# Kernel optimization log

Hardware: AMD Instinct MI355X
Metric: run time of the kernel (lower is better)

The kernel has to match this reference:

```python
import jax, jax.numpy as jnp
import numpy as np

B, D_IN, FD = 32768, 2048, 128
N1 = N2 = N3 = 4
T = 1.0  # temperature buffer value (eval mode)
LN_EPS = 1e-5

def _gelu(x):
    return jax.nn.gelu(x, approximate=False)  # torch nn.GELU default = exact erf

def setup_inputs() -> dict:
    key = jax.random.key(0)
    ks = iter(jax.random.split(key, 64))
    def rn(shape, s=0.02):
        return jax.random.normal(next(ks), shape, jnp.float32) * s
    inp = {"x": jax.random.normal(next(ks), (B, D_IN), jnp.float32)}
    # input_proj: Linear(2048,512) GELU Linear(512,256) LayerNorm(256)
    inp.update(ipW1=rn((D_IN, 512)), ipb1=jnp.zeros(512), ipW2=rn((512, 256)), ipb2=jnp.zeros(256),
               ln_g=jnp.ones(256), ln_b=jnp.zeros(256))
    def level(din, nc, pfx):
        return {pfx+"W3d": rn((din, 3)), pfx+"b3d": jnp.zeros(3),
                pfx+"c": rn((nc, 3), 0.3), pfx+"lr": jnp.zeros(nc),
                pfx+"f1W": rn((din, FD)), pfx+"f1b": jnp.zeros(FD),
                pfx+"f2W": rn((FD, FD)), pfx+"f2b": jnp.zeros(FD),
                pfx+"rW": rn((FD+3, nc)), pfx+"rb": jnp.zeros(nc)}
    inp.update(level(256, N1, "l1"))
    inp.update(level(FD, N2, "l2"))
    inp.update(level(FD, N3, "l3"))
    # expert_head: Linear(128+4+4+4, 256) GELU Linear(256, 64)
    inp.update(ehW1=rn((FD+N1+N2+N3, 256)), ehb1=jnp.zeros(256),
               ehW2=rn((256, N1*N2*N3)), ehb2=jnp.zeros(N1*N2*N3))
    return inp

def _level_fwd(x, W3d, b3d, c, f1W, f1b, f2W, f2b, rW, rb):
    # x: (B, din) -> probs (B, nc), features (B, FD)
    pos = x @ W3d + b3d                                   # (B, 3)
    d_sq = ((pos[:, None, :] - c[None, :, :]) ** 2).sum(-1)  # (B, nc)
    geo = -d_sq / (2.0 * T * T + 1e-8)                    # non-spectral geo signal
    feat = _gelu(x @ f1W + f1b) @ f2W + f2b               # (B, FD)
    logits = jnp.concatenate([feat, pos], axis=-1) @ rW + rb + 0.5 * geo
    probs = jax.nn.softmax(logits / max(T, 0.1), axis=-1)  # eval path: plain softmax
    return probs, feat

def _router_fwd(x, ipW1, ipb1, ipW2, ipb2, ln_g, ln_b,
                l1W3d, l1b3d, l1c, l1f1W, l1f1b, l1f2W, l1f2b, l1rW, l1rb,
                l2W3d, l2b3d, l2c, l2f1W, l2f1b, l2f2W, l2f2b, l2rW, l2rb,
                l3W3d, l3b3d, l3c, l3f1W, l3f1b, l3f2W, l3f2b, l3rW, l3rb,
                ehW1, ehb1, ehW2, ehb2):
    h = _gelu(x @ ipW1 + ipb1) @ ipW2 + ipb2
    mu = h.mean(-1, keepdims=True)
    var = ((h - mu) ** 2).mean(-1, keepdims=True)
    h = (h - mu) * jax.lax.rsqrt(var + LN_EPS) * ln_g + ln_b  # LayerNorm(256)
    p1, f1 = _level_fwd(h,  l1W3d, l1b3d, l1c, l1f1W, l1f1b, l1f2W, l1f2b, l1rW, l1rb)
    p2, f2 = _level_fwd(f1, l2W3d, l2b3d, l2c, l2f1W, l2f1b, l2f2W, l2f2b, l2rW, l2rb)
    p3, f3 = _level_fwd(f2, l3W3d, l3b3d, l3c, l3f1W, l3f1b, l3f2W, l3f2b, l3rW, l3rb)
    combined = jnp.concatenate([f3, p1, p2, p3], axis=-1)  # (B, 140)
    logits = _gelu(combined @ ehW1 + ehb1) @ ehW2 + ehb2   # (B, 64)
    expert_probs = jax.nn.softmax(logits / max(T, 0.1), axis=-1)
    return expert_probs

def reference(x, ipW1, ipb1, ipW2, ipb2, ln_g, ln_b,
              l1W3d, l1b3d, l1c, l1lr, l1f1W, l1f1b, l1f2W, l1f2b, l1rW, l1rb,
              l2W3d, l2b3d, l2c, l2lr, l2f1W, l2f1b, l2f2W, l2f2b, l2rW, l2rb,
              l3W3d, l3b3d, l3c, l3lr, l3f1W, l3f1b, l3f2W, l3f2b, l3rW, l3rb,
              ehW1, ehb1, ehW2, ehb2):
    # l?lr (log_radii) are unused in non-spectral mode, matching the source.
    expert_probs = _router_fwd(x, ipW1, ipb1, ipW2, ipb2, ln_g, ln_b,
                               l1W3d, l1b3d, l1c, l1f1W, l1f1b, l1f2W, l1f2b, l1rW, l1rb,
                               l2W3d, l2b3d, l2c, l2f1W, l2f1b, l2f2W, l2f2b, l2rW, l2rb,
                               l3W3d, l3b3d, l3c, l3f1W, l3f1b, l3f2W, l3f2b, l3rW, l3rb,
                               ehW1, ehb1, ehW2, ehb2)
    expert_ids = jnp.argmax(expert_probs, axis=-1)
    return expert_probs, expert_ids
```

## Files before the change

kernel.cpp:

```cpp
#include <hip/hip_runtime.h>
#include <hip/hip_bf16.h>
#include <cstdint>
#include <cstddef>


typedef short  s8v  __attribute__((ext_vector_type(8)));
typedef float  f4v  __attribute__((ext_vector_type(4)));
typedef float  f16v __attribute__((ext_vector_type(16)));
typedef unsigned int u32;

#define B_ROWS 32768

__device__ inline short f2bf(float x) {
    __hip_bfloat16 h = __float2bfloat16(x);
    return __builtin_bit_cast(short, h);
}
__device__ inline float bf2f(short s) {
    return __bfloat162float(__builtin_bit_cast(__hip_bfloat16, s));
}
__device__ inline float gelu_f(float x) {
    return 0.5f * x * (1.0f + erff(x * 0.70710678118654752440f));
}
__device__ inline void gload_lds16(const short* g, short* l) {
    __builtin_amdgcn_global_load_lds(
        (const __attribute__((address_space(1))) u32*)g,
        (__attribute__((address_space(3))) u32*)l, 16, 0, 0);
}

__global__ void split_w1_img(const float* __restrict__ W, short* __restrict__ img)
{
    const int idx = blockIdx.x * 256 + threadIdx.x;
    const int p = idx & 7;
    const int n = (idx >> 3) & 511;
    const int t = idx >> 12;
    const int cs = p ^ (n & 7);
    const int plane = cs >> 2, kc = cs & 3;
    const int kbase = t * 32 + kc * 8;
    s8v v8;
    #pragma unroll
    for (int e = 0; e < 8; ++e) {
        const float v = W[(size_t)(kbase + e) * 512 + n];
        const short h = f2bf(v);
        v8[e] = plane ? f2bf(v - bf2f(h)) : h;
    }
    *(s8v*)&img[(size_t)((t * 512 + n) * 64 + p * 8)] = v8;
}

__launch_bounds__(256, 4)
__global__ void gemm1k(const float* __restrict__ X,
                       const short* __restrict__ Bimg,
                       const float* __restrict__ bias,
                       float* __restrict__ out)
{
    __shared__ short smem[128 * 64 * 2];
    short* Ab = smem;
    short* Bb = smem + 128 * 64;

    const int tid = threadIdx.x;
    const int l = tid & 63, wid = tid >> 6;
    const int wr = wid >> 1, wc = wid & 1;

    const int d = blockIdx.x;
    const int xcd = d & 7;
    const int m0 = ((xcd & 1) * 128 + (d >> 3)) * 128;
    const int n0 = (xcd >> 1) * 128;

    const int ar = tid & 127, ah = tid >> 7;
    const float* xP = X + (size_t)(m0 + ar) * 2048 + ah * 16;
    short* awr = Ab + ar * 64;
    const int pw0 = ((ah * 2    ) ^ (ar & 7)) * 8;
    const int pw1 = ((ah * 2 + 1) ^ (ar & 7)) * 8;
    const int pw2 = ((ah * 2 + 4) ^ (ar & 7)) * 8;
    const int pw3 = ((ah * 2 + 5) ^ (ar & 7)) * 8;

    const short* bP = Bimg + (size_t)n0 * 64 + (size_t)(wid * 4) * 512 + (size_t)l * 8;
    short* bD = Bb + wid * 4 * 512;

    f16v acc[2][2];
    #pragma unroll
    for (int m = 0; m < 2; ++m)
        #pragma unroll
        for (int n = 0; n < 2; ++n) acc[m][n] = (f16v)0.0f;

    f4v cur0, cur1, cur2, cur3;
    cur0 = *(const f4v*)(xP + 0);
    cur1 = *(const f4v*)(xP + 4);
    cur2 = *(const f4v*)(xP + 8);
    cur3 = *(const f4v*)(xP + 12);

    for (int t = 0; t < 64; ++t) {
        s8v hi0, hi1, lo0, lo1;
        #pragma unroll
        for (int e = 0; e < 4; ++e) {
            float v;
            short h;
            v = cur0[e]; h = f2bf(v); hi0[e]     = h; lo0[e]     = f2bf(v - bf2f(h));
            v = cur1[e]; h = f2bf(v); hi0[e + 4] = h; lo0[e + 4] = f2bf(v - bf2f(h));
            v = cur2[e]; h = f2bf(v); hi1[e]     = h; lo1[e]     = f2bf(v - bf2f(h));
            v = cur3[e]; h = f2bf(v); hi1[e + 4] = h; lo1[e + 4] = f2bf(v - bf2f(h));
        }
        __syncthreads();
        *(s8v*)&awr[pw0] = hi0;
        *(s8v*)&awr[pw1] = hi1;
        *(s8v*)&awr[pw2] = lo0;
        *(s8v*)&awr[pw3] = lo1;
        {
            const short* bt = bP + (size_t)t * 32768;
            gload_lds16(bt,          bD);
            gload_lds16(bt +  512,   bD + 512);
            gload_lds16(bt + 1024,   bD + 1024);
            gload_lds16(bt + 1536,   bD + 1536);
        }
        if (t < 63) {
            const float* p = xP + (t + 1) * 32;
            cur0 = *(const f4v*)(p + 0);
            cur1 = *(const f4v*)(p + 4);
            cur2 = *(const f4v*)(p + 8);
            cur3 = *(const f4v*)(p + 12);
        }
        __syncthreads();

        #pragma unroll
        for (int ks = 0; ks < 2; ++ks) {
            const int ph0 = ks * 2 + (l >> 5);
            s8v ahf[2], alf[2], bhf[2], blf[2];
            #pragma unroll
            for (int m = 0; m < 2; ++m) {
                const int row = wr * 64 + m * 32 + (l & 31);
                const int ph = ph0 ^ (row & 7);
                ahf[m] = *(const s8v*)&Ab[row * 64 + ph * 8];
                alf[m] = *(const s8v*)&Ab[row * 64 + (ph ^ 4) * 8];
            }
            #pragma unroll
            for (int n = 0; n < 2; ++n) {
                const int col = wc * 64 + n * 32 + (l & 31);
                const int ph = ph0 ^ (col & 7);
                bhf[n] = *(const s8v*)&Bb[col * 64 + ph * 8];
                blf[n] = *(const s8v*)&Bb[col * 64 + (ph ^ 4) * 8];
            }
            #pragma unroll
            for (int m = 0; m < 2; ++m)
                #pragma unroll
                for (int n = 0; n < 2; ++n) {
                    acc[m][n] = __builtin_amdgcn_mfma_f32_32x32x16_bf16(ahf[m], bhf[n], acc[m][n], 0, 0, 0);
                    acc[m][n] = __builtin_amdgcn_mfma_f32_32x32x16_bf16(ahf[m], blf[n], acc[m][n], 0, 0, 0);
                    acc[m][n] = __builtin_amdgcn_mfma_f32_32x32x16_bf16(alf[m], bhf[n], acc[m][n], 0, 0, 0);
                }
        }
    }

    #pragma unroll
    for (int m = 0; m < 2; ++m) {
        #pragma unroll
        for (int n = 0; n < 2; ++n) {
            const int gcol = n0 + wc * 64 + n * 32 + (l & 31);
            const float bv = bias[gcol];
            #pragma unroll
            for (int r = 0; r < 16; ++r) {
                const int grow = m0 + wr * 64 + m * 32
                               + (r & 3) + 8 * (r >> 2) + 4 * (l >> 5);
                out[(size_t)grow * 512 + gcol] = gelu_f(acc[m][n][r] + bv);
            }
        }
    }
}

struct SplitDesc { const float* W; short* dst; int K, N, Kpad, blk0; };
struct SplitPack { SplitDesc d[9]; };

__global__ void split_all(SplitPack p) {
    const int bid = blockIdx.x;
    int i = 0;
    #pragma unroll
    for (int j = 1; j < 9; ++j) if (bid >= p.d[j].blk0) i = j;
    const SplitDesc& D = p.d[i];
    const int idx = (bid - D.blk0) * 256 + threadIdx.x;
    const int total = D.N * D.Kpad;
    if (idx >= total) return;
    const int n = idx / D.Kpad, k = idx - n * D.Kpad;
    const float v = (k < D.K) ? D.W[(size_t)k * D.N + n] : 0.0f;
    const short hs = f2bf(v);
    D.dst[idx] = hs;
    D.dst[total + idx] = f2bf(v - bf2f(hs));
}

template<int DIN, int OSTR>
__launch_bounds__(256, 2)
__global__ void levelk(const float* __restrict__ X,
                       const short* __restrict__ Wa, const float* __restrict__ ba,
                       const short* __restrict__ Wb, const float* __restrict__ bb,
                       float* __restrict__ F)
{
    constexpr int NT1 = DIN / 32;
    __shared__ short stepb[(64 + 128) * 64];
    __shared__ float gb[64 * 132];
    short* Ab = stepb;
    short* Bb = stepb + 64 * 64;

    const int tid = threadIdx.x;
    const int l = tid & 63, wid = tid >> 6;
    const int wr = wid >> 1, wc = wid & 1;
    const int m0 = blockIdx.x * 64;

    const int ar = tid >> 2, aseg = tid & 3;
    short* aw = Ab + ar * 64;
    const int ps0 = ((aseg    ) ^ (ar & 7)) * 8;
    const int ps1 = ((aseg + 4) ^ (ar & 7)) * 8;

    const int cs = (l & 7) ^ (l >> 3);
    const int bplane = cs >> 2, kslot = cs & 3;

    f16v acc[2];
    acc[0] = (f16v)0.0f; acc[1] = (f16v)0.0f;

    auto computeStep = [&]() {
        #pragma unroll
        for (int ks = 0; ks < 2; ++ks) {
            const int c0 = ks * 2 + (l >> 5);
            const int row = wr * 32 + (l & 31);
            const int pa = c0 ^ (row & 7);
            s8v ah = *(const s8v*)&Ab[row * 64 + pa * 8];
            s8v al = *(const s8v*)&Ab[row * 64 + (pa ^ 4) * 8];
            #pragma unroll
            for (int n = 0; n < 2; ++n) {
                const int col = wc * 64 + n * 32 + (l & 31);
                const int pb = c0 ^ (col & 7);
                s8v bh = *(const s8v*)&Bb[col * 64 + pb * 8];
                s8v bl = *(const s8v*)&Bb[col * 64 + (pb ^ 4) * 8];
                acc[n] = __builtin_amdgcn_mfma_f32_32x32x16_bf16(ah, bh, acc[n], 0, 0, 0);
                acc[n] = __builtin_amdgcn_mfma_f32_32x32x16_bf16(ah, bl, acc[n], 0, 0, 0);
                acc[n] = __builtin_amdgcn_mfma_f32_32x32x16_bf16(al, bh, acc[n], 0, 0, 0);
            }
        }
    };
    auto cvt = [&](const f4v& u, const f4v& w, s8v& hi, s8v& lo) {
        #pragma unroll
        for (int e = 0; e < 4; ++e) {
            short h;
            h = f2bf(u[e]); hi[e]     = h; lo[e]     = f2bf(u[e] - bf2f(h));
            h = f2bf(w[e]); hi[e + 4] = h; lo[e + 4] = f2bf(w[e] - bf2f(h));
        }
    };

    {
        const float* xP = X + (size_t)(m0 + ar) * DIN + aseg * 8;
        f4v cA = *(const f4v*)(xP);
        f4v cB = *(const f4v*)(xP + 4);
        for (int t = 0; t < NT1; ++t) {
            s8v hi, lo; cvt(cA, cB, hi, lo);
            __syncthreads();
            *(s8v*)&aw[ps0] = hi;
            *(s8v*)&aw[ps1] = lo;
            #pragma unroll
            for (int j = 0; j < 4; ++j) {
                const int col = (wid * 4 + j) * 8 + (l >> 3);
                gload_lds16(Wa + (size_t)bplane * (128 * DIN) + (size_t)col * DIN
                               + t * 32 + kslot * 8,
                            Bb + (wid * 4 + j) * 512);
            }
            if (t + 1 < NT1) {
                const float* p = xP + (t + 1) * 32;
                cA = *(const f4v*)(p);
                cB = *(const f4v*)(p + 4);
            }
            __syncthreads();
            computeStep();
        }
    }

    #pragma unroll
    for (int n = 0; n < 2; ++n) {
        const int col = wc * 64 + n * 32 + (l & 31);
        const float bv = ba[col];
        #pragma unroll
        for (int r = 0; r < 16; ++r) {
            const int row = wr * 32 + (r & 3) + 8 * (r >> 2) + 4 * (l >> 5);
            gb[row * 132 + col] = gelu_f(acc[n][r] + bv);
        }
    }
    acc[0] = (f16v)0.0f; acc[1] = (f16v)0.0f;
    __syncthreads();

    {
        const float* gP = gb + ar * 132 + aseg * 8;
        f4v cA = *(const f4v*)(gP);
        f4v cB = *(const f4v*)(gP + 4);
        for (int t = 0; t < 4; ++t) {
            s8v hi, lo; cvt(cA, cB, hi, lo);
            __syncthreads();
            *(s8v*)&aw[ps0] = hi;
            *(s8v*)&aw[ps1] = lo;
            #pragma unroll
            for (int j = 0; j < 4; ++j) {
                const int col = (wid * 4 + j) * 8 + (l >> 3);
                gload_lds16(Wb + (size_t)bplane * (128 * 128) + (size_t)col * 128
                               + t * 32 + kslot * 8,
                            Bb + (wid * 4 + j) * 512);
            }
            if (t + 1 < 4) {
                const float* p = gP + (t + 1) * 32;
                cA = *(const f4v*)(p);
                cB = *(const f4v*)(p + 4);
            }
            __syncthreads();
            computeStep();
        }
    }

    #pragma unroll
    for (int n = 0; n < 2; ++n) {
        const int col = wc * 64 + n * 32 + (l & 31);
        const float bv = bb[col];
        #pragma unroll
        for (int r = 0; r < 16; ++r) {
            const int row = wr * 32 + (r & 3) + 8 * (r >> 2) + 4 * (l >> 5);
            F[(size_t)(m0 + row) * OSTR + col] = acc[n][r] + bv;
        }
    }
}

template<int BM, int BN, int EPI>
__launch_bounds__(256, 2)
__global__ void gemm32(const float* __restrict__ A, int lda,
                       const short* __restrict__ Bsp, int ldb, int NK,
                       const float* __restrict__ bias, int K, int N, int ntiles,
                       float* __restrict__ out, float* __restrict__ out2,
                       const float* __restrict__ lng, const float* __restrict__ lnb)
{
    constexpr int MF  = BM / 64;
    constexpr int NFw = BN / 64;
    constexpr int BUF = (BM + BN) * 64;
    constexpr int FPT = BM / 8;
    constexpr int TPR = 32 / FPT;
    constexpr int nBI = BN / 32;
    __shared__ short smem[2 * BUF];

    const int tid = threadIdx.x;
    const int l   = tid & 63, wid = tid >> 6;
    const int wr  = wid >> 1, wc = wid & 1;
    const int bid = blockIdx.x;
    const int ntb = bid % ntiles, mtb = bid / ntiles;
    const int m0  = mtb * BM, n0 = ntb * BN;

    const int ar = tid / TPR, aseg = tid % TPR;
    const float* aP = A + (size_t)(m0 + ar) * lda + aseg * FPT;

    const short* bg[nBI];
    {
        const int cs = (l & 7) ^ (l >> 3);
        const int plane = cs >> 2, kslot = cs & 3;
        #pragma unroll
        for (int j = 0; j < nBI; ++j) {
            const int col = (wid * nBI + j) * 8 + (l >> 3);
            bg[j] = Bsp + (size_t)plane * NK + (size_t)(n0 + col) * ldb + kslot * 8;
        }
    }

    f16v acc[MF][NFw];
    #pragma unroll
    for (int m = 0; m < MF; ++m)
        #pragma unroll
        for (int n = 0; n < NFw; ++n) acc[m][n] = (f16v)0.0f;

    f4v areg[FPT / 4];

    auto loadA = [&](int t) {
        const float* p = aP + t * 32;
        #pragma unroll
        for (int i = 0; i < FPT / 4; ++i) areg[i] = *(const f4v*)(p + i * 4);
    };
    auto stageB = [&](int t, short* buf) {
        short* Bb = buf + BM * 64;
        #pragma unroll
        for (int j = 0; j < nBI; ++j)
            gload_lds16(bg[j] + t * 32, Bb + (wid * nBI + j) * 512);
    };
    auto writeA = [&](short* buf) {
        #pragma unroll
        for (int c = 0; c < FPT / 8; ++c) {
            s8v hi, lo;
            #pragma unroll
            for (int e = 0; e < 8; ++e) {
                const float v = areg[c * 2 + (e >> 2)][e & 3];
                const short hs = f2bf(v);
                hi[e] = hs; lo[e] = f2bf(v - bf2f(hs));
            }
            const int csh = aseg * (FPT / 8) + c;
            *(s8v*)&buf[ar * 64 + ((csh    ) ^ (ar & 7)) * 8] = hi;
            *(s8v*)&buf[ar * 64 + ((csh + 4) ^ (ar & 7)) * 8] = lo;
        }
    };
    auto compute = [&](const short* buf) {
        const short* Ab = buf;
        const short* Bb = buf + BM * 64;
        #pragma unroll
        for (int ks = 0; ks < 2; ++ks) {
            const int csb = ks * 2 + (l >> 5);
            s8v ah[MF], al[MF], bh[NFw], bl[NFw];
            #pragma unroll
            for (int m = 0; m < MF; ++m) {
                const int row = wr * (BM / 2) + m * 32 + (l & 31);
                ah[m] = *(const s8v*)&Ab[row * 64 + ((csb    ) ^ (row & 7)) * 8];
                al[m] = *(const s8v*)&Ab[row * 64 + ((csb + 4) ^ (row & 7)) * 8];
            }
            #pragma unroll
            for (int n = 0; n < NFw; ++n) {
                const int col = wc * (BN / 2) + n * 32 + (l & 31);
                bh[n] = *(const s8v*)&Bb[col * 64 + ((csb    ) ^ (col & 7)) * 8];
                bl[n] = *(const s8v*)&Bb[col * 64 + ((csb + 4) ^ (col & 7)) * 8];
            }
            __builtin_amdgcn_s_setprio(1);
            #pragma unroll
            for (int m = 0; m < MF; ++m)
                #pragma unroll
                for (int n = 0; n < NFw; ++n) {
                    acc[m][n] = __builtin_amdgcn_mfma_f32_32x32x16_bf16(ah[m], bh[n], acc[m][n], 0, 0, 0);
                    acc[m][n] = __builtin_amdgcn_mfma_f32_32x32x16_bf16(ah[m], bl[n], acc[m][n], 0, 0, 0);
                    acc[m][n] = __builtin_amdgcn_mfma_f32_32x32x16_bf16(al[m], bh[n], acc[m][n], 0, 0, 0);
                }
            __builtin_amdgcn_s_setprio(0);
        }
    };

    const int NT = K / 32;
    loadA(0);
    stageB(0, smem);
    writeA(smem);
    __syncthreads();
    for (int t = 0; t < NT; ++t) {
        short* curb = smem + (t & 1) * BUF;
        short* nxtb = smem + ((t & 1) ^ 1) * BUF;
        const bool pf = (t + 1 < NT);
        if (pf) { loadA(t + 1); stageB(t + 1, nxtb); }
        compute(curb);
        if (pf) writeA(nxtb);
        __syncthreads();
    }

    if constexpr (EPI <= 1) {
        #pragma unroll
        for (int m = 0; m < MF; ++m) {
            #pragma unroll
            for (int n = 0; n < NFw; ++n) {
                const int gcol = n0 + wc * (BN / 2) + n * 32 + (l & 31);
                const float bv = bias[gcol];
                #pragma unroll
                for (int r = 0; r < 16; ++r) {
                    const int grow = m0 + wr * (BM / 2) + m * 32
                                   + (r & 3) + 8 * (r >> 2) + 4 * (l >> 5);
                    float xv = acc[m][n][r] + bv;
                    if constexpr (EPI == 0) xv = gelu_f(xv);
                    out[(size_t)grow * N + gcol] = xv;
                }
            }
        }
    } else if constexpr (EPI == 2) {
        float* LT = reinterpret_cast<float*>(smem);
        const int gcolL = wc * 32 + (l & 31);
        const float bv = bias[gcolL];
        #pragma unroll
        for (int r = 0; r < 16; ++r) {
            const int row = wr * 32 + (r & 3) + 8 * (r >> 2) + 4 * (l >> 5);
            LT[row * 64 + gcolL] = acc[0][0][r] + bv;
        }
        __syncthreads();
        const int r = tid >> 2, q = tid & 3;
        const float* Lr = LT + r * 64 + q * 16;
        float mx = Lr[0];
        #pragma unroll
        for (int c = 1; c < 16; ++c) mx = fmaxf(mx, Lr[c]);
        mx = fmaxf(mx, __shfl_xor(mx, 1));
        mx = fmaxf(mx, __shfl_xor(mx, 2));
        float ev[16]; float s = 0.0f;
        #pragma unroll
        for (int c = 0; c < 16; ++c) { ev[c] = expf(Lr[c] - mx); s += ev[c]; }
        s += __shfl_xor(s, 1);
        s += __shfl_xor(s, 2);
        float pmax = -1.0f; int arg = 0;
        #pragma unroll
        for (int c = 0; c < 16; ++c) {
            const float pv = ev[c] / s;
            out[(size_t)(m0 + r) * 64 + q * 16 + c] = pv;
            if (pv > pmax) { pmax = pv; arg = q * 16 + c; }
        }
        #pragma unroll
        for (int off = 1; off <= 2; off <<= 1) {
            const float po = __shfl_xor(pmax, off);
            const int   ao = __shfl_xor(arg, off);
            if (po > pmax || (po == pmax && ao < arg)) { pmax = po; arg = ao; }
        }
        if (q == 0) out2[m0 + r] = (float)arg;
    } else {
        float* LT = reinterpret_cast<float*>(smem);
        #pragma unroll
        for (int n = 0; n < NFw; ++n) {
            const int col = wc * (BN / 2) + n * 32 + (l & 31);
            const float bv = bias[col];
            #pragma unroll
            for (int r = 0; r < 16; ++r) {
                const int row = wr * 32 + (r & 3) + 8 * (r >> 2) + 4 * (l >> 5);
                LT[row * 264 + col] = acc[0][n][r] + bv;
            }
        }
        __syncthreads();
        const int r = tid >> 2, q = tid & 3;
        const float* Lr = LT + r * 264 + q * 64;
        float s = 0.0f;
        #pragma unroll
        for (int i = 0; i < 64; ++i) s += Lr[i];
        s += __shfl_xor(s, 1);
        s += __shfl_xor(s, 2);
        const float mu = s * 0.00390625f;
        float qv = 0.0f;
        #pragma unroll
        for (int i = 0; i < 64; ++i) { const float dd = Lr[i] - mu; qv += dd * dd; }
        qv += __shfl_xor(qv, 1);
        qv += __shfl_xor(qv, 2);
        const float sc = 1.0f / sqrtf(qv * 0.00390625f + 1e-5f);
        #pragma unroll
        for (int i = 0; i < 64; ++i) {
            const int c = q * 64 + i;
            out[(size_t)(m0 + r) * 256 + c] = (Lr[i] - mu) * sc * lng[c] + lnb[c];
        }
    }
}

__global__ __launch_bounds__(256) void p_kernel(
    const float* __restrict__ X, int din,
    const float* __restrict__ F, int fstr,
    const float* __restrict__ W3d, const float* __restrict__ b3d,
    const float* __restrict__ cc,
    const float* __restrict__ rW, const float* __restrict__ rb,
    float* __restrict__ Pout)
{
    const int row = blockIdx.x * 4 + (threadIdx.x >> 6);
    const int l   = threadIdx.x & 63;
    float px0 = 0.f, px1 = 0.f, px2 = 0.f;
    const int per = din >> 6;
    const float* xr = X + (size_t)row * din;
    for (int i = 0; i < per; ++i) {
        const int k = l + (i << 6);
        const float xv = xr[k];
        px0 += xv * W3d[k*3 + 0];
        px1 += xv * W3d[k*3 + 1];
        px2 += xv * W3d[k*3 + 2];
    }
    float g0 = 0.f, g1 = 0.f, g2 = 0.f, g3 = 0.f;
    const float* fr = F + (size_t)row * fstr;
    #pragma unroll
    for (int i = 0; i < 2; ++i) {
        const int k = l + (i << 6);
        const float fv = fr[k];
        g0 += fv * rW[k*4 + 0]; g1 += fv * rW[k*4 + 1];
        g2 += fv * rW[k*4 + 2]; g3 += fv * rW[k*4 + 3];
    }
    #pragma unroll
    for (int o = 32; o; o >>= 1) {
        px0 += __shfl_xor(px0, o); px1 += __shfl_xor(px1, o); px2 += __shfl_xor(px2, o);
        g0  += __shfl_xor(g0, o);  g1  += __shfl_xor(g1, o);
        g2  += __shfl_xor(g2, o);  g3  += __shfl_xor(g3, o);
    }
    if (l == 0) {
        const float pos0 = px0 + b3d[0], pos1 = px1 + b3d[1], pos2 = px2 + b3d[2];
        float lg[4];
        float mx = -1e30f;
        float gg[4] = {g0, g1, g2, g3};
        #pragma unroll
        for (int c = 0; c < 4; ++c) {
            float a = gg[c] + rb[c]
                    + pos0 * rW[512 + c] + pos1 * rW[516 + c] + pos2 * rW[520 + c];
            const float d0 = pos0 - cc[c*3 + 0];
            const float d1 = pos1 - cc[c*3 + 1];
            const float d2 = pos2 - cc[c*3 + 2];
            a += 0.5f * (-(d0*d0 + d1*d1 + d2*d2) / 2.00000001f);
            lg[c] = a;
            mx = fmaxf(mx, a);
        }
        const float e0 = expf(lg[0]-mx), e1 = expf(lg[1]-mx),
                    e2 = expf(lg[2]-mx), e3 = expf(lg[3]-mx);
        const float s = e0 + e1 + e2 + e3;
        float* pr = Pout + (size_t)row * 160;
        pr[0] = e0/s; pr[1] = e1/s; pr[2] = e2/s; pr[3] = e3/s;
    }
}

extern "C" void kernel_launch(void* const* d_in, const int* in_sizes, int n_in,
                              void* d_out, int out_size, void* d_ws, size_t ws_size,
                              hipStream_t stream)
{
    (void)in_sizes; (void)n_in; (void)out_size; (void)ws_size;

    const float* x    = (const float*)d_in[0];
    const float* ipW1 = (const float*)d_in[1];
    const float* ipb1 = (const float*)d_in[2];
    const float* ipW2 = (const float*)d_in[3];
    const float* ipb2 = (const float*)d_in[4];
    const float* ln_g = (const float*)d_in[5];
    const float* ln_b = (const float*)d_in[6];
    const float* W3d[3] = {(const float*)d_in[7],  (const float*)d_in[17], (const float*)d_in[27]};
    const float* b3d[3] = {(const float*)d_in[8],  (const float*)d_in[18], (const float*)d_in[28]};
    const float* cc[3]  = {(const float*)d_in[9],  (const float*)d_in[19], (const float*)d_in[29]};
    const float* f1W[3] = {(const float*)d_in[11], (const float*)d_in[21], (const float*)d_in[31]};
    const float* f1b[3] = {(const float*)d_in[12], (const float*)d_in[22], (const float*)d_in[32]};
    const float* f2W[3] = {(const float*)d_in[13], (const float*)d_in[23], (const float*)d_in[33]};
    const float* f2b[3] = {(const float*)d_in[14], (const float*)d_in[24], (const float*)d_in[34]};
    const float* rW[3]  = {(const float*)d_in[15], (const float*)d_in[25], (const float*)d_in[35]};
    const float* rb[3]  = {(const float*)d_in[16], (const float*)d_in[26], (const float*)d_in[36]};
    const float* ehW1 = (const float*)d_in[37];
    const float* ehb1 = (const float*)d_in[38];
    const float* ehW2 = (const float*)d_in[39];
    const float* ehb2 = (const float*)d_in[40];

    size_t off = 0;
    auto take = [&](size_t bytes) -> void* {
        void* p = (char*)d_ws + off;
        off += (bytes + 255) & ~(size_t)255;
        return p;
    };
    auto takeW = [&](int N, int Kpad) -> short* {
        return (short*)take((size_t)2 * N * Kpad * 2);
    };
    short* W1img = (short*)take((size_t)64 * 512 * 64 * 2);
    short* W2s = takeW(256, 512);
    short* L1a = takeW(128, 256);
    short* L1b = takeW(128, 128);
    short* L2a = takeW(128, 128);
    short* L2b = takeW(128, 128);
    short* L3a = takeW(128, 128);
    short* L3b = takeW(128, 128);
    short* E1s = takeW(256, 160);
    short* E2s = takeW(64, 256);
    float* h1 = (float*)take((size_t)B_ROWS * 512 * 4);
    float* h2 = (float*)take((size_t)B_ROWS * 256 * 4);
    float* f1 = (float*)take((size_t)B_ROWS * 128 * 4);
    float* f2 = (float*)take((size_t)B_ROWS * 128 * 4);
    float* comb = h1;
    float* geh  = (float*)((char*)h1 + ((size_t)22 << 20));

    split_w1_img<<<(64 * 512 * 8) / 256, 256, 0, stream>>>(ipW1, W1img);
    SplitPack sp;
    int blk = 0;
    auto desc = [&](int i, const float* W, short* dst, int K, int N, int Kpad) {
        sp.d[i] = {W, dst, K, N, Kpad, blk};
        blk += (N * Kpad + 255) / 256;
    };
    desc(0, ipW2,   W2s,  512, 256,  512);
    desc(1, f1W[0], L1a,  256, 128,  256);
    desc(2, f2W[0], L1b,  128, 128,  128);
    desc(3, f1W[1], L2a,  128, 128,  128);
    desc(4, f2W[1], L2b,  128, 128,  128);
    desc(5, f1W[2], L3a,  128, 128,  128);
    desc(6, f2W[2], L3b,  128, 128,  128);
    desc(7, ehW1,   E1s,  140, 256,  160);
    desc(8, ehW2,   E2s,  256,  64,  256);
    split_all<<<blk, 256, 0, stream>>>(sp);

    const dim3 blkT(256);
    constexpr int MG64 = B_ROWS / 64;

    gemm1k<<<1024, blkT, 0, stream>>>(x, W1img, ipb1, h1);
    gemm32<64,256,3><<<MG64, blkT, 0, stream>>>(h1, 512, W2s, 512, 256*512, ipb2,
                                                512, 256, 1, h2, nullptr, ln_g, ln_b);

    levelk<256,128><<<MG64, blkT, 0, stream>>>(h2, L1a, f1b[0], L1b, f2b[0], f1);
    p_kernel<<<B_ROWS/4, 256, 0, stream>>>(h2, 256, f1, 128, W3d[0], b3d[0], cc[0], rW[0], rb[0], comb + 128);
    levelk<128,128><<<MG64, blkT, 0, stream>>>(f1, L2a, f1b[1], L2b, f2b[1], f2);
    p_kernel<<<B_ROWS/4, 256, 0, stream>>>(f1, 128, f2, 128, W3d[1], b3d[1], cc[1], rW[1], rb[1], comb + 132);
    levelk<128,160><<<MG64, blkT, 0, stream>>>(f2, L3a, f1b[2], L3b, f2b[2], comb);
    p_kernel<<<B_ROWS/4, 256, 0, stream>>>(f2, 128, comb, 160, W3d[2], b3d[2], cc[2], rW[2], rb[2], comb + 136);

    gemm32<64,128,0><<<MG64*2, blkT, 0, stream>>>(comb, 160, E1s, 160, 256*160, ehb1,
                                                  160, 256, 2, geh, nullptr, nullptr, nullptr);
    gemm32<64,64,2><<<MG64, blkT, 0, stream>>>(geh, 256, E2s, 256, 64*256, ehb2,
                                               256, 64, 1, (float*)d_out,
                                               (float*)d_out + (size_t)B_ROWS * 64, nullptr, nullptr);
}
```

Baseline: 555.5 us.

## Fuse all three router levels and expert-head first layer into one megakernel

Replaces the three levelk launches, three p_kernel launches and the first expert-head GEMM with a single per-64-row kernel. Intermediate features, position/probability results and the combined vector stay in LDS instead of going through global memory. Separately, the second input-projection GEMM now uses a 128x128 tile with a plain bias epilogue, followed by a standalone vectorized LayerNorm kernel instead of the fused LN epilogue. This removes launch overhead and global round-trips between stages, at the cost of heavy register use (a 16-vector register cache of the input row), large LDS usage that may limit occupancy, and an extra pass over h2 for LayerNorm.

New measurement: 538.9 us. -3.0%, faster.

```diff
diff --git a/kernel.cpp b/kernel.cpp
--- a/kernel.cpp
+++ b/kernel.cpp
@@ -10,6 +10,8 @@
 typedef unsigned int u32;
 
 #define B_ROWS 32768
+
+template<int N> struct IC { static constexpr int v = N; };
 
 __device__ inline short f2bf(float x) {
     __hip_bfloat16 h = __float2bfloat16(x);
@@ -184,148 +186,12 @@
     D.dst[total + idx] = f2bf(v - bf2f(hs));
 }
 
-template<int DIN, int OSTR>
-__launch_bounds__(256, 2)
-__global__ void levelk(const float* __restrict__ X,
-                       const short* __restrict__ Wa, const float* __restrict__ ba,
-                       const short* __restrict__ Wb, const float* __restrict__ bb,
-                       float* __restrict__ F)
-{
-    constexpr int NT1 = DIN / 32;
-    __shared__ short stepb[(64 + 128) * 64];
-    __shared__ float gb[64 * 132];
-    short* Ab = stepb;
-    short* Bb = stepb + 64 * 64;
-
-    const int tid = threadIdx.x;
-    const int l = tid & 63, wid = tid >> 6;
-    const int wr = wid >> 1, wc = wid & 1;
-    const int m0 = blockIdx.x * 64;
-
-    const int ar = tid >> 2, aseg = tid & 3;
-    short* aw = Ab + ar * 64;
-    const int ps0 = ((aseg    ) ^ (ar & 7)) * 8;
-    const int ps1 = ((aseg + 4) ^ (ar & 7)) * 8;
-
-    const int cs = (l & 7) ^ (l >> 3);
-    const int bplane = cs >> 2, kslot = cs & 3;
-
-    f16v acc[2];
-    acc[0] = (f16v)0.0f; acc[1] = (f16v)0.0f;
-
-    auto computeStep = [&]() {
-        #pragma unroll
-        for (int ks = 0; ks < 2; ++ks) {
-            const int c0 = ks * 2 + (l >> 5);
-            const int row = wr * 32 + (l & 31);
-            const int pa = c0 ^ (row & 7);
-            s8v ah = *(const s8v*)&Ab[row * 64 + pa * 8];
-            s8v al = *(const s8v*)&Ab[row * 64 + (pa ^ 4) * 8];
-            #pragma unroll
-            for (int n = 0; n < 2; ++n) {
-                const int col = wc * 64 + n * 32 + (l & 31);
-                const int pb = c0 ^ (col & 7);
-                s8v bh = *(const s8v*)&Bb[col * 64 + pb * 8];
-                s8v bl = *(const s8v*)&Bb[col * 64 + (pb ^ 4) * 8];
-                acc[n] = __builtin_amdgcn_mfma_f32_32x32x16_bf16(ah, bh, acc[n], 0, 0, 0);
-                acc[n] = __builtin_amdgcn_mfma_f32_32x32x16_bf16(ah, bl, acc[n], 0, 0, 0);
-                acc[n] = __builtin_amdgcn_mfma_f32_32x32x16_bf16(al, bh, acc[n], 0, 0, 0);
-            }
-        }
-    };
-    auto cvt = [&](const f4v& u, const f4v& w, s8v& hi, s8v& lo) {
-        #pragma unroll
-        for (int e = 0; e < 4; ++e) {
-            short h;
-            h = f2bf(u[e]); hi[e]     = h; lo[e]     = f2bf(u[e] - bf2f(h));
-            h = f2bf(w[e]); hi[e + 4] = h; lo[e + 4] = f2bf(w[e] - bf2f(h));
-        }
-    };
-
-    {
-        const float* xP = X + (size_t)(m0 + ar) * DIN + aseg * 8;
-        f4v cA = *(const f4v*)(xP);
-        f4v cB = *(const f4v*)(xP + 4);
-        for (int t = 0; t < NT1; ++t) {
-            s8v hi, lo; cvt(cA, cB, hi, lo);
-            __syncthreads();
-            *(s8v*)&aw[ps0] = hi;
-            *(s8v*)&aw[ps1] = lo;
-            #pragma unroll
-            for (int j = 0; j < 4; ++j) {
-                const int col = (wid * 4 + j) * 8 + (l >> 3);
-                gload_lds16(Wa + (size_t)bplane * (128 * DIN) + (size_t)col * DIN
-                               + t * 32 + kslot * 8,
-                            Bb + (wid * 4 + j) * 512);
-            }
-            if (t + 1 < NT1) {
-                const float* p = xP + (t + 1) * 32;
-                cA = *(const f4v*)(p);
-                cB = *(const f4v*)(p + 4);
-            }
-            __syncthreads();
-            computeStep();
-        }
-    }
-
-    #pragma unroll
-    for (int n = 0; n < 2; ++n) {
-        const int col = wc * 64 + n * 32 + (l & 31);
-        const float bv = ba[col];
-        #pragma unroll
-        for (int r = 0; r < 16; ++r) {
-            const int row = wr * 32 + (r & 3) + 8 * (r >> 2) + 4 * (l >> 5);
-            gb[row * 132 + col] = gelu_f(acc[n][r] + bv);
-        }
-    }
-    acc[0] = (f16v)0.0f; acc[1] = (f16v)0.0f;
-    __syncthreads();
-
-    {
-        const float* gP = gb + ar * 132 + aseg * 8;
-        f4v cA = *(const f4v*)(gP);
-        f4v cB = *(const f4v*)(gP + 4);
-        for (int t = 0; t < 4; ++t) {
-            s8v hi, lo; cvt(cA, cB, hi, lo);
-            __syncthreads();
-            *(s8v*)&aw[ps0] = hi;
-            *(s8v*)&aw[ps1] = lo;
-            #pragma unroll
-            for (int j = 0; j < 4; ++j) {
-                const int col = (wid * 4 + j) * 8 + (l >> 3);
-                gload_lds16(Wb + (size_t)bplane * (128 * 128) + (size_t)col * 128
-                               + t * 32 + kslot * 8,
-                            Bb + (wid * 4 + j) * 512);
-            }
-            if (t + 1 < 4) {
-                const float* p = gP + (t + 1) * 32;
-                cA = *(const f4v*)(p);
-                cB = *(const f4v*)(p + 4);
-            }
-            __syncthreads();
-            computeStep();
-        }
-    }
-
-    #pragma unroll
-    for (int n = 0; n < 2; ++n) {
-        const int col = wc * 64 + n * 32 + (l & 31);
-        const float bv = bb[col];
-        #pragma unroll
-        for (int r = 0; r < 16; ++r) {
-            const int row = wr * 32 + (r & 3) + 8 * (r >> 2) + 4 * (l >> 5);
-            F[(size_t)(m0 + row) * OSTR + col] = acc[n][r] + bv;
-        }
-    }
-}
-
 template<int BM, int BN, int EPI>
 __launch_bounds__(256, 2)
 __global__ void gemm32(const float* __restrict__ A, int lda,
                        const short* __restrict__ Bsp, int ldb, int NK,
                        const float* __restrict__ bias, int K, int N, int ntiles,
-                       float* __restrict__ out, float* __restrict__ out2,
-                       const float* __restrict__ lng, const float* __restrict__ lnb)
+                       float* __restrict__ out, float* __restrict__ out2)
 {
     constexpr int MF  = BM / 64;
     constexpr int NFw = BN / 64;
@@ -454,7 +320,7 @@
                 }
             }
         }
-    } else if constexpr (EPI == 2) {
+    } else {
         float* LT = reinterpret_cast<float*>(smem);
         const int gcolL = wc * 32 + (l & 31);
         const float bv = bias[gcolL];
@@ -490,97 +356,290 @@
             if (po > pmax || (po == pmax && ao < arg)) { pmax = po; arg = ao; }
         }
         if (q == 0) out2[m0 + r] = (float)arg;
-    } else {
-        float* LT = reinterpret_cast<float*>(smem);
-        #pragma unroll
-        for (int n = 0; n < NFw; ++n) {
-            const int col = wc * (BN / 2) + n * 32 + (l & 31);
-            const float bv = bias[col];
-            #pragma unroll
-            for (int r = 0; r < 16; ++r) {
-                const int row = wr * 32 + (r & 3) + 8 * (r >> 2) + 4 * (l >> 5);
-                LT[row * 264 + col] = acc[0][n][r] + bv;
-            }
-        }
-        __syncthreads();
-        const int r = tid >> 2, q = tid & 3;
-        const float* Lr = LT + r * 264 + q * 64;
-        float s = 0.0f;
-        #pragma unroll
-        for (int i = 0; i < 64; ++i) s += Lr[i];
-        s += __shfl_xor(s, 1);
-        s += __shfl_xor(s, 2);
-        const float mu = s * 0.00390625f;
-        float qv = 0.0f;
-        #pragma unroll
-        for (int i = 0; i < 64; ++i) { const float dd = Lr[i] - mu; qv += dd * dd; }
-        qv += __shfl_xor(qv, 1);
-        qv += __shfl_xor(qv, 2);
-        const float sc = 1.0f / sqrtf(qv * 0.00390625f + 1e-5f);
-        #pragma unroll
-        for (int i = 0; i < 64; ++i) {
-            const int c = q * 64 + i;
-            out[(size_t)(m0 + r) * 256 + c] = (Lr[i] - mu) * sc * lng[c] + lnb[c];
-        }
-    }
-}
-
-__global__ __launch_bounds__(256) void p_kernel(
-    const float* __restrict__ X, int din,
-    const float* __restrict__ F, int fstr,
-    const float* __restrict__ W3d, const float* __restrict__ b3d,
-    const float* __restrict__ cc,
-    const float* __restrict__ rW, const float* __restrict__ rb,
-    float* __restrict__ Pout)
+    }
+}
+
+__global__ __launch_bounds__(256) void ln_kernel(float* __restrict__ H,
+                                                 const float* __restrict__ G,
+                                                 const float* __restrict__ Bv)
 {
     const int row = blockIdx.x * 4 + (threadIdx.x >> 6);
     const int l   = threadIdx.x & 63;
-    float px0 = 0.f, px1 = 0.f, px2 = 0.f;
-    const int per = din >> 6;
-    const float* xr = X + (size_t)row * din;
-    for (int i = 0; i < per; ++i) {
-        const int k = l + (i << 6);
-        const float xv = xr[k];
-        px0 += xv * W3d[k*3 + 0];
-        px1 += xv * W3d[k*3 + 1];
-        px2 += xv * W3d[k*3 + 2];
-    }
-    float g0 = 0.f, g1 = 0.f, g2 = 0.f, g3 = 0.f;
-    const float* fr = F + (size_t)row * fstr;
-    #pragma unroll
-    for (int i = 0; i < 2; ++i) {
-        const int k = l + (i << 6);
-        const float fv = fr[k];
-        g0 += fv * rW[k*4 + 0]; g1 += fv * rW[k*4 + 1];
-        g2 += fv * rW[k*4 + 2]; g3 += fv * rW[k*4 + 3];
-    }
-    #pragma unroll
-    for (int o = 32; o; o >>= 1) {
-        px0 += __shfl_xor(px0, o); px1 += __shfl_xor(px1, o); px2 += __shfl_xor(px2, o);
-        g0  += __shfl_xor(g0, o);  g1  += __shfl_xor(g1, o);
-        g2  += __shfl_xor(g2, o);  g3  += __shfl_xor(g3, o);
-    }
-    if (l == 0) {
-        const float pos0 = px0 + b3d[0], pos1 = px1 + b3d[1], pos2 = px2 + b3d[2];
-        float lg[4];
-        float mx = -1e30f;
-        float gg[4] = {g0, g1, g2, g3};
-        #pragma unroll
-        for (int c = 0; c < 4; ++c) {
-            float a = gg[c] + rb[c]
-                    + pos0 * rW[512 + c] + pos1 * rW[516 + c] + pos2 * rW[520 + c];
-            const float d0 = pos0 - cc[c*3 + 0];
-            const float d1 = pos1 - cc[c*3 + 1];
-            const float d2 = pos2 - cc[c*3 + 2];
-            a += 0.5f * (-(d0*d0 + d1*d1 + d2*d2) / 2.00000001f);
-            lg[c] = a;
-            mx = fmaxf(mx, a);
-        }
-        const float e0 = expf(lg[0]-mx), e1 = expf(lg[1]-mx),
-                    e2 = expf(lg[2]-mx), e3 = expf(lg[3]-mx);
-        const float s = e0 + e1 + e2 + e3;
-        float* pr = Pout + (size_t)row * 160;
-        pr[0] = e0/s; pr[1] = e1/s; pr[2] = e2/s; pr[3] = e3/s;
+    float* hr = H + (size_t)row * 256;
+    f4v v = *reinterpret_cast<const f4v*>(&hr[l * 4]);
+    float s = v[0] + v[1] + v[2] + v[3];
+    #pragma unroll
+    for (int o = 32; o; o >>= 1) s += __shfl_xor(s, o);
+    const float mu = s * 0.00390625f;
+    f4v d = v - mu;
+    float q = d[0]*d[0] + d[1]*d[1] + d[2]*d[2] + d[3]*d[3];
+    #pragma unroll
+    for (int o = 32; o; o >>= 1) q += __shfl_xor(q, o);
+    const float var = q * 0.00390625f;
+    const float sc  = 1.0f / sqrtf(var + 1e-5f);
+    f4v gg = *reinterpret_cast<const f4v*>(&G[l * 4]);
+    f4v bb = *reinterpret_cast<const f4v*>(&Bv[l * 4]);
+    f4v o4 = d * sc * gg + bb;
+    *reinterpret_cast<f4v*>(&hr[l * 4]) = o4;
+}
+
+struct TailArgs {
+    const float* h2;
+    const short* La[3]; const float* ba[3];
+    const short* Lb[3]; const float* bb[3];
+    const short* E1;    const float* eb1;
+    const float* W3d[3]; const float* b3d[3]; const float* cc[3];
+    const float* rW[3];  const float* rb[3];
+    float* geh;
+};
+
+__launch_bounds__(256, 2)
+__global__ void megatail(TailArgs A)
+{
+    __shared__ float Fbuf[64 * 164];
+    __shared__ short Astage[64 * 64];
+    __shared__ short Bstage[128 * 64];
+    __shared__ float pbuf[64 * 12];
+
+    const int tid = threadIdx.x;
+    const int l = tid & 63, wid = tid >> 6;
+    const int wr = wid >> 1, wc = wid & 1;
+    const int m0 = blockIdx.x * 64;
+
+    const int ar = tid >> 2, aseg = tid & 3;
+    short* aw = Astage + ar * 64;
+    const int ps0 = ((aseg    ) ^ (ar & 7)) * 8;
+    const int ps1 = ((aseg + 4) ^ (ar & 7)) * 8;
+
+    const int cs = (l & 7) ^ (l >> 3);
+    const int bplane = cs >> 2, kslot = cs & 3;
+
+    f16v acc[2];
+
+    auto accReset = [&]() { acc[0] = (f16v)0.0f; acc[1] = (f16v)0.0f; };
+
+    auto computeStep = [&]() {
+        #pragma unroll
+        for (int ks = 0; ks < 2; ++ks) {
+            const int c0 = ks * 2 + (l >> 5);
+            const int row = wr * 32 + (l & 31);
+            const int pa = c0 ^ (row & 7);
+            s8v ah = *(const s8v*)&Astage[row * 64 + pa * 8];
+            s8v al = *(const s8v*)&Astage[row * 64 + (pa ^ 4) * 8];
+            #pragma unroll
+            for (int n = 0; n < 2; ++n) {
+                const int col = wc * 64 + n * 32 + (l & 31);
+                const int pb = c0 ^ (col & 7);
+                s8v bh = *(const s8v*)&Bstage[col * 64 + pb * 8];
+                s8v bl = *(const s8v*)&Bstage[col * 64 + (pb ^ 4) * 8];
+                acc[n] = __builtin_amdgcn_mfma_f32_32x32x16_bf16(ah, bh, acc[n], 0, 0, 0);
+                acc[n] = __builtin_amdgcn_mfma_f32_32x32x16_bf16(ah, bl, acc[n], 0, 0, 0);
+                acc[n] = __builtin_amdgcn_mfma_f32_32x32x16_bf16(al, bh, acc[n], 0, 0, 0);
+            }
+        }
+    };
+    auto cvt = [&](const f4v& u, const f4v& w, s8v& hi, s8v& lo) {
+        #pragma unroll
+        for (int e = 0; e < 4; ++e) {
+            short h;
+            h = f2bf(u[e]); hi[e]     = h; lo[e]     = f2bf(u[e] - bf2f(h));
+            h = f2bf(w[e]); hi[e + 4] = h; lo[e + 4] = f2bf(w[e] - bf2f(h));
+        }
+    };
+    auto stageBt = [&](const short* Bpl, int Kpad, int NKpl, int n0, int t) {
+        #pragma unroll
+        for (int j = 0; j < 4; ++j) {
+            const int col = (wid * 4 + j) * 8 + (l >> 3);
+            gload_lds16(Bpl + (size_t)bplane * NKpl + (size_t)(n0 + col) * Kpad
+                            + t * 32 + kslot * 8,
+                        Bstage + (wid * 4 + j) * 512);
+        }
+    };
+
+    auto phaseRegs = [&](auto NTc, const f4v* xr, const short* Bpl, int Kpad, int NKpl) {
+        constexpr int NT = decltype(NTc)::v;
+        #pragma unroll
+        for (int t = 0; t < NT; ++t) {
+            s8v hi, lo; cvt(xr[2 * t], xr[2 * t + 1], hi, lo);
+            __syncthreads();
+            *(s8v*)&aw[ps0] = hi;
+            *(s8v*)&aw[ps1] = lo;
+            stageBt(Bpl, Kpad, NKpl, 0, t);
+            __syncthreads();
+            computeStep();
+        }
+    };
+    auto phaseLDS = [&](auto NTc, const short* Bpl, int Kpad, int NKpl, int n0) {
+        constexpr int NT = decltype(NTc)::v;
+        f4v cA = *(const f4v*)&Fbuf[ar * 164 + aseg * 8];
+        f4v cB = *(const f4v*)&Fbuf[ar * 164 + aseg * 8 + 4];
+        #pragma unroll
+        for (int t = 0; t < NT; ++t) {
+            s8v hi, lo; cvt(cA, cB, hi, lo);
+            __syncthreads();
+            *(s8v*)&aw[ps0] = hi;
+            *(s8v*)&aw[ps1] = lo;
+            stageBt(Bpl, Kpad, NKpl, n0, t);
+            if (t + 1 < NT) {
+                cA = *(const f4v*)&Fbuf[ar * 164 + (t + 1) * 32 + aseg * 8];
+                cB = *(const f4v*)&Fbuf[ar * 164 + (t + 1) * 32 + aseg * 8 + 4];
+            }
+            __syncthreads();
+            computeStep();
+        }
+    };
+    auto outEpi = [&](const float* bv_arr, bool dogelu) {
+        #pragma unroll
+        for (int n = 0; n < 2; ++n) {
+            const int col = wc * 64 + n * 32 + (l & 31);
+            const float bv = bv_arr[col];
+            #pragma unroll
+            for (int r = 0; r < 16; ++r) {
+                const int row = wr * 32 + (r & 3) + 8 * (r >> 2) + 4 * (l >> 5);
+                float xv = acc[n][r] + bv;
+                if (dogelu) xv = gelu_f(xv);
+                Fbuf[row * 164 + col] = xv;
+            }
+        }
+    };
+    auto pComp = [&](auto NSLc, const f4v* xr, const float* W3dG, const float* b3dG,
+                     const float* ccG, const float* rWG, const float* rbG, int pidx) {
+        constexpr int NSL = decltype(NSLc)::v;
+        float* Cs = (float*)Bstage;
+        __syncthreads();
+        for (int i = tid; i < NSL * 32 * 3; i += 256) Cs[i] = W3dG[i];
+        for (int i = tid; i < 131 * 4;      i += 256) Cs[1024 + i] = rWG[i];
+        if (tid < 12) Cs[1600 + tid] = ccG[tid];
+        if (tid < 3)  Cs[1616 + tid] = b3dG[tid];
+        if (tid < 4)  Cs[1620 + tid] = rbG[tid];
+        __syncthreads();
+        float p0 = 0.f, p1 = 0.f, p2 = 0.f;
+        #pragma unroll
+        for (int t = 0; t < NSL; ++t)
+            #pragma unroll
+            for (int e = 0; e < 8; ++e) {
+                const int k = t * 32 + aseg * 8 + e;
+                const float v = (e < 4) ? xr[2 * t][e] : xr[2 * t + 1][e - 4];
+                p0 += v * Cs[k * 3 + 0];
+                p1 += v * Cs[k * 3 + 1];
+                p2 += v * Cs[k * 3 + 2];
+            }
+        float g0 = 0.f, g1 = 0.f, g2 = 0.f, g3 = 0.f;
+        #pragma unroll
+        for (int i = 0; i < 32; ++i) {
+            const int k = aseg * 32 + i;
+            const float f = Fbuf[ar * 164 + k];
+            g0 += f * Cs[1024 + k * 4 + 0];
+            g1 += f * Cs[1024 + k * 4 + 1];
+            g2 += f * Cs[1024 + k * 4 + 2];
+            g3 += f * Cs[1024 + k * 4 + 3];
+        }
+        #pragma unroll
+        for (int o = 1; o <= 2; o <<= 1) {
+            p0 += __shfl_xor(p0, o); p1 += __shfl_xor(p1, o); p2 += __shfl_xor(p2, o);
+            g0 += __shfl_xor(g0, o); g1 += __shfl_xor(g1, o);
+            g2 += __shfl_xor(g2, o); g3 += __shfl_xor(g3, o);
+        }
+        if (aseg == 0) {
+            const float pos0 = p0 + Cs[1616], pos1 = p1 + Cs[1617], pos2 = p2 + Cs[1618];
+            float lg[4];
+            float gg[4] = {g0, g1, g2, g3};
+            float mx = -1e30f;
+            #pragma unroll
+            for (int c = 0; c < 4; ++c) {
+                float a = gg[c] + Cs[1620 + c]
+                        + pos0 * Cs[1024 + 128 * 4 + c]
+                        + pos1 * Cs[1024 + 129 * 4 + c]
+                        + pos2 * Cs[1024 + 130 * 4 + c];
+                const float d0 = pos0 - Cs[1600 + c * 3 + 0];
+                const float d1 = pos1 - Cs[1600 + c * 3 + 1];
+                const float d2 = pos2 - Cs[1600 + c * 3 + 2];
+                a += 0.5f * (-(d0 * d0 + d1 * d1 + d2 * d2) / 2.00000001f);
+                lg[c] = a;
+                mx = fmaxf(mx, a);
+            }
+            const float e0 = expf(lg[0] - mx), e1 = expf(lg[1] - mx),
+                        e2 = expf(lg[2] - mx), e3 = expf(lg[3] - mx);
+            const float s = e0 + e1 + e2 + e3;
+            float* pr = pbuf + ar * 12 + pidx * 4;
+            pr[0] = e0 / s; pr[1] = e1 / s; pr[2] = e2 / s; pr[3] = e3 / s;
+        }
+    };
+
+    f4v x1[16];
+    {
+        const float* xp = A.h2 + (size_t)(m0 + ar) * 256 + aseg * 8;
+        #pragma unroll
+        for (int t = 0; t < 8; ++t) {
+            x1[2 * t]     = *(const f4v*)(xp + t * 32);
+            x1[2 * t + 1] = *(const f4v*)(xp + t * 32 + 4);
+        }
+    }
+    accReset();
+    phaseRegs(IC<8>{}, x1, A.La[0], 256, 128 * 256);
+    outEpi(A.ba[0], true);
+    accReset();
+    __syncthreads();
+    phaseLDS(IC<4>{}, A.Lb[0], 128, 128 * 128, 0);
+    outEpi(A.bb[0], false);
+    pComp(IC<8>{}, x1, A.W3d[0], A.b3d[0], A.cc[0], A.rW[0], A.rb[0], 0);
+
+    f4v x2[8];
+    #pragma unroll
+    for (int t = 0; t < 4; ++t) {
+        x2[2 * t]     = *(const f4v*)&Fbuf[ar * 164 + t * 32 + aseg * 8];
+        x2[2 * t + 1] = *(const f4v*)&Fbuf[ar * 164 + t * 32 + aseg * 8 + 4];
+    }
+    accReset();
+    phaseRegs(IC<4>{}, x2, A.La[1], 128, 128 * 128);
+    outEpi(A.ba[1], true);
+    accReset();
+    __syncthreads();
+    phaseLDS(IC<4>{}, A.Lb[1], 128, 128 * 128, 0);
+    outEpi(A.bb[1], false);
+    pComp(IC<4>{}, x2, A.W3d[1], A.b3d[1], A.cc[1], A.rW[1], A.rb[1], 1);
+
+    f4v x3[8];
+    #pragma unroll
+    for (int t = 0; t < 4; ++t) {
+        x3[2 * t]     = *(const f4v*)&Fbuf[ar * 164 + t * 32 + aseg * 8];
+        x3[2 * t + 1] = *(const f4v*)&Fbuf[ar * 164 + t * 32 + aseg * 8 + 4];
+    }
+    accReset();
+    phaseRegs(IC<4>{}, x3, A.La[2], 128, 128 * 128);
+    outEpi(A.ba[2], true);
+    accReset();
+    __syncthreads();
+    phaseLDS(IC<4>{}, A.Lb[2], 128, 128 * 128, 0);
+    outEpi(A.bb[2], false);
+    pComp(IC<4>{}, x3, A.W3d[2], A.b3d[2], A.cc[2], A.rW[2], A.rb[2], 2);
+
+    __syncthreads();
+    {
+        const int row = tid >> 2, base = (tid & 3) * 9;
+        #pragma unroll
+        for (int jj = 0; jj < 9; ++jj) {
+            const int col = 128 + base + jj;
+            Fbuf[row * 164 + col] = (col < 140) ? pbuf[row * 12 + (col - 128)] : 0.0f;
+        }
+    }
+    __syncthreads();
+
+    #pragma unroll
+    for (int nh = 0; nh < 2; ++nh) {
+        accReset();
+        phaseLDS(IC<5>{}, A.E1, 160, 256 * 160, nh * 128);
+        #pragma unroll
+        for (int n = 0; n < 2; ++n) {
+            const int col = nh * 128 + wc * 64 + n * 32 + (l & 31);
+            const float bv = A.eb1[col];
+            #pragma unroll
+            for (int r = 0; r < 16; ++r) {
+                const int row = wr * 32 + (r & 3) + 8 * (r >> 2) + 4 * (l >> 5);
+                A.geh[(size_t)(m0 + row) * 256 + col] = gelu_f(acc[n][r] + bv);
+            }
+        }
+        if (nh == 0) __syncthreads();
     }
 }
 
@@ -630,12 +689,9 @@
     short* L3b = takeW(128, 128);
     short* E1s = takeW(256, 160);
     short* E2s = takeW(64, 256);
-    float* h1 = (float*)take((size_t)B_ROWS * 512 * 4);
-    float* h2 = (float*)take((size_t)B_ROWS * 256 * 4);
-    float* f1 = (float*)take((size_t)B_ROWS * 128 * 4);
-    float* f2 = (float*)take((size_t)B_ROWS * 128 * 4);
-    float* comb = h1;
-    float* geh  = (float*)((char*)h1 + ((size_t)22 << 20));
+    float* h1  = (float*)take((size_t)B_ROWS * 512 * 4);
+    float* h2  = (float*)take((size_t)B_ROWS * 256 * 4);
+    float* geh = (float*)take((size_t)B_ROWS * 256 * 4);
 
     split_w1_img<<<(64 * 512 * 8) / 256, 256, 0, stream>>>(ipW1, W1img);
     SplitPack sp;
@@ -659,19 +715,25 @@
     constexpr int MG64 = B_ROWS / 64;
 
     gemm1k<<<1024, blkT, 0, stream>>>(x, W1img, ipb1, h1);
-    gemm32<64,256,3><<<MG64, blkT, 0, stream>>>(h1, 512, W2s, 512, 256*512, ipb2,
-                                                512, 256, 1, h2, nullptr, ln_g, ln_b);
-
-    levelk<256,128><<<MG64, blkT, 0, stream>>>(h2, L1a, f1b[0], L1b, f2b[0], f1);
-    p_kernel<<<B_ROWS/4, 256, 0, stream>>>(h2, 256, f1, 128, W3d[0], b3d[0], cc[0], rW[0], rb[0], comb + 128);
-    levelk<128,128><<<MG64, blkT, 0, stream>>>(f1, L2a, f1b[1], L2b, f2b[1], f2);
-    p_kernel<<<B_ROWS/4, 256, 0, stream>>>(f1, 128, f2, 128, W3d[1], b3d[1], cc[1], rW[1], rb[1], comb + 132);
-    levelk<128,160><<<MG64, blkT, 0, stream>>>(f2, L3a, f1b[2], L3b, f2b[2], comb);
-    p_kernel<<<B_ROWS/4, 256, 0, stream>>>(f2, 128, comb, 160, W3d[2], b3d[2], cc[2], rW[2], rb[2], comb + 136);
-
-    gemm32<64,128,0><<<MG64*2, blkT, 0, stream>>>(comb, 160, E1s, 160, 256*160, ehb1,
-                                                  160, 256, 2, geh, nullptr, nullptr, nullptr);
+    gemm32<128,128,1><<<(B_ROWS/128)*2, blkT, 0, stream>>>(h1, 512, W2s, 512, 256*512,
+                                                           ipb2, 512, 256, 2, h2, nullptr);
+    ln_kernel<<<B_ROWS/4, 256, 0, stream>>>(h2, ln_g, ln_b);
+
+    TailArgs ta;
+    ta.h2 = h2;
+    ta.La[0] = L1a; ta.La[1] = L2a; ta.La[2] = L3a;
+    ta.Lb[0] = L1b; ta.Lb[1] = L2b; ta.Lb[2] = L3b;
+    ta.ba[0] = f1b[0]; ta.ba[1] = f1b[1]; ta.ba[2] = f1b[2];
+    ta.bb[0] = f2b[0]; ta.bb[1] = f2b[1]; ta.bb[2] = f2b[2];
+    ta.E1 = E1s; ta.eb1 = ehb1;
+    for (int i = 0; i < 3; ++i) {
+        ta.W3d[i] = W3d[i]; ta.b3d[i] = b3d[i]; ta.cc[i] = cc[i];
+        ta.rW[i] = rW[i];   ta.rb[i] = rb[i];
+    }
+    ta.geh = geh;
+    megatail<<<MG64, blkT, 0, stream>>>(ta);
+
     gemm32<64,64,2><<<MG64, blkT, 0, stream>>>(geh, 256, E2s, 256, 64*256, ehb2,
                                                256, 64, 1, (float*)d_out,
-                                               (float*)d_out + (size_t)B_ROWS * 64, nullptr, nullptr);
-}
+                                               (float*)d_out + (size_t)B_ROWS * 64);
+}
```
